# Optimization experiments

Hardware: AMD Instinct MI355X
Metric: run time of the kernel (lower is better)

Reference implementation:

```python
import jax, jax.numpy as jnp
import numpy as np

N = 768          # n_nuclei
EMB = 32         # embedding_dim
RBF = 32         # rbf_dim
CUTOFF = 10.0    # rbf_cutoff
MAXQ = 10        # max(charges)


def _edges(n):
    # fully-connected edge list exactly as in GNN.__call__
    senders = np.arange(n).repeat(n - 1)
    recv = np.arange(n)[None].repeat(n - 1, axis=0)
    recv = (recv + np.arange(n - 1)[:, None] + 1) % n
    return jnp.asarray(senders), jnp.asarray(recv.reshape(-1))


def _mlp2(x, w0, b0, w1, b1=None):
    # AutoMLP(out_dim, depth=2): Dense+silu, Dense (final_bias optional)
    h = jax.nn.silu(x @ w0 + b0)
    y = h @ w1
    return y if b1 is None else y + b1


def _seg_mean(vals, seg, n):
    s = jax.ops.segment_sum(vals, seg, num_segments=n, indices_are_sorted=True)
    c = jax.ops.segment_sum(jnp.ones((vals.shape[0], 1), vals.dtype), seg,
                            num_segments=n, indices_are_sorted=True)
    return s / jnp.maximum(c, 1.0)


def setup_inputs() -> dict:
    key = jax.random.key(0)
    ki = iter(jax.random.split(key, 48))

    def W(din, dout):
        return jax.random.normal(next(ki), (din, dout), jnp.float32) / np.sqrt(din).astype(np.float32)

    def b(d):
        return jax.random.normal(next(ki), (d,), jnp.float32) * 0.01

    return dict(
        nuclei=jax.random.normal(next(ki), (N, 3), jnp.float32) * 3.0,
        charges=jax.random.randint(next(ki), (N,), 0, MAXQ),
        f=(jnp.arange(RBF, dtype=jnp.float32) + 1.0) * jnp.pi,  # BesselRBF param init
        embed_table=jax.random.normal(next(ki), (MAXQ, EMB), jnp.float32),
        mp1_w0=W(96, 32), mp1_b0=b(32), mp1_w1=W(32, 32), mp1_b1=b(32),
        up1_w0=W(64, 64), up1_b0=b(64), up1_w1=W(64, 64), up1_b1=b(64),
        mp2_w0=W(160, 32), mp2_b0=b(32), mp2_w1=W(32, 32), mp2_b1=b(32),
        up2_w0=W(96, 64), up2_b0=b(64), up2_w1=W(64, 64), up2_b1=b(64),
        no_w0=W(160, 3), no_b0=b(3), no_w1=W(3, 3),
        no_embed=jax.random.normal(next(ki), (MAXQ, 3), jnp.float32) * 0.1,
        go_w0=W(160, 1), go_b0=b(1), go_w1=W(1, 1), go_b1=b(1),
    )


def reference(nuclei, charges, f, embed_table,
              mp1_w0, mp1_b0, mp1_w1, mp1_b1,
              up1_w0, up1_b0, up1_w1, up1_b1,
              mp2_w0, mp2_b0, mp2_w1, mp2_b1,
              up2_w0, up2_b0, up2_w1, up2_b1,
              no_w0, no_b0, no_w1, no_embed,
              go_w0, go_b0, go_w1, go_b1):
    nuclei = nuclei.reshape(-1, 3) @ jnp.eye(3, dtype=nuclei.dtype)  # constants 'axes'
    n = nuclei.shape[0]
    senders, receivers = _edges(n)

    # BesselRBF on pairwise distances
    d = jnp.linalg.norm(nuclei[senders] - nuclei[receivers], axis=-1)
    x_ext = d[:, None] + 1e-8
    e_embed = jnp.sqrt(2.0 / CUTOFF) * jnp.sin(f * x_ext / CUTOFF) / x_ext  # [E, RBF]

    n_embed = embed_table[charges]  # [N, EMB]
    embeddings = [n_embed]

    # layer 1: msg out 32, update out 64 (no residual: 32 != 64)
    edge_in = jnp.concatenate([n_embed[senders], n_embed[receivers], e_embed], axis=-1)
    msg = _seg_mean(_mlp2(edge_in, mp1_w0, mp1_b0, mp1_w1, mp1_b1), senders, n)
    upd = _mlp2(jnp.concatenate([n_embed, msg], axis=-1), up1_w0, up1_b0, up1_w1, up1_b1)
    n_embed = upd  # dims differ -> plain replacement
    embeddings.append(n_embed)

    # layer 2: msg out 32, update out 64 (residual: 64 == 64)
    edge_in = jnp.concatenate([n_embed[senders], n_embed[receivers], e_embed], axis=-1)
    msg = _seg_mean(_mlp2(edge_in, mp2_w0, mp2_b0, mp2_w1, mp2_b1), senders, n)
    upd = _mlp2(jnp.concatenate([n_embed, msg], axis=-1), up2_w0, up2_b0, up2_w1, up2_b1)
    n_embed = n_embed + upd
    embeddings.append(n_embed)

    agg = jnp.concatenate(embeddings, axis=-1)  # [N, 32+64+64=160]

    node_out = _mlp2(agg, no_w0, no_b0, no_w1) + no_embed[charges]  # [N, 3]
    global_out = _mlp2(jnp.mean(agg, axis=0), go_w0, go_b0, go_w1, go_b1)  # [1]
    return (node_out, global_out)
```

## Files before the change

kernel.cpp:

```cpp
#include <hip/hip_runtime.h>
#include <hip/hip_bf16.h>

typedef __hip_bfloat16 bf16;
typedef __attribute__((ext_vector_type(8))) short short8;
typedef __attribute__((ext_vector_type(4))) float float4v;

#define NN   768
#define NEPS 767

__device__ float g_emb1[NN*64];
__device__ float g_sa2[NN*32];
__device__ float g_sb2[NN*32];
__device__ float g_agg[640];
__device__ int   g_cnt;

struct Ptrs { const void* p[28]; };

__device__ __forceinline__ float b2f(bf16 v){ return __bfloat162float(v); }
__device__ __forceinline__ float LD(const void* p, int i, int f32){
  return f32 ? ((const float*)p)[i] : b2f(((const bf16*)p)[i]);
}
__device__ __forceinline__ int detect_f32(const void* f){
  float v = ((const float*)f)[0];
  return (fabsf(v - 3.14159265f) < 0.01f) ? 1 : 0;
}
__device__ __forceinline__ float fast_rcp(float x){ return __builtin_amdgcn_rcpf(x); }
__device__ __forceinline__ float silu_f(float p){ return p * fast_rcp(1.f + __expf(-p)); }
__device__ __forceinline__ unsigned short rne_bf16(float x){
  unsigned int b = __float_as_uint(x);
  return (unsigned short)((b + 0x7fffu + ((b >> 16) & 1u)) >> 16);
}

template<int NJ>
__device__ __forceinline__ float dotn(const void* wp, int base, int stride, int col,
                                      const float* x, int k0, int isf){
  float p = 0.f;
  if (isf){
    const float* f = (const float*)wp;
    #pragma unroll
    for (int j = 0; j < NJ; j++){ int k = k0 + j; p = fmaf(x[k], f[base + k*stride + col], p); }
  } else {
    const bf16* h = (const bf16*)wp;
    #pragma unroll
    for (int j = 0; j < NJ; j++){ int k = k0 + j; p = fmaf(x[k], b2f(h[base + k*stride + col]), p); }
  }
  return p;
}

__launch_bounds__(256)
__global__ void k_edge1(Ptrs P, const int* __restrict__ charges){
  __shared__ __align__(16) float pos[NN*3];
  __shared__ float etabL[320];
  __shared__ __align__(16) float w0F[2048];
  __shared__ float TBL[330];
  __shared__ int   chS[NN];
  __shared__ float w1L[1024];
  __shared__ float wsum[4][32], hsumL[32], msgL[32];
  __shared__ float catU[64], hU[64], e1U[64], part[256];

  int i = blockIdx.x, t = threadIdx.x;
  int w = t >> 6, lane = t & 63, q = lane >> 4, c = lane & 15;
  int isf = detect_f32(P.p[2]);

  if (i == 0){
    for (int idx = t; idx < 640; idx += 256) g_agg[idx] = 0.f;
    if (t == 0) g_cnt = 0;
  }
  for (int idx = t; idx < NN*3; idx += 256) pos[idx]   = LD(P.p[0], idx, isf);
  for (int idx = t; idx < 320;  idx += 256) etabL[idx] = LD(P.p[3], idx, isf);
  for (int idx = t; idx < 2048; idx += 256) w0F[idx]   = LD(P.p[4], idx, isf);
  for (int idx = t; idx < 1024; idx += 256) w1L[idx]   = LD(P.p[6], idx, isf);
  for (int idx = t; idx < NN;   idx += 256) chS[idx]   = charges[idx];

  short8 bfr0, bfr1;
  if (isf){
    const float* wp = (const float*)P.p[4];
    #pragma unroll
    for (int j = 0; j < 8; j++){
      int row = q*8 + j;
      bfr0[j] = (short)rne_bf16(wp[2048 + row*32 + c]);
      bfr1[j] = (short)rne_bf16(wp[2048 + row*32 + 16 + c]);
    }
  } else {
    const short* wp = (const short*)P.p[4];
    #pragma unroll
    for (int j = 0; j < 8; j++){
      int row = q*8 + j;
      bfr0[j] = wp[2048 + row*32 + c];
      bfr1[j] = wp[2048 + row*32 + 16 + c];
    }
  }
  float fj[8];
  #pragma unroll
  for (int j = 0; j < 8; j++) fj[j] = LD(P.p[2], q*8 + j, isf) * 0.1f;
  __syncthreads();

  for (int idx = t; idx < 320; idx += 256){
    int ch = idx >> 5, cc = idx & 31;
    float b = 0.f;
    #pragma unroll
    for (int k = 0; k < 32; k++) b = fmaf(etabL[ch*32 + k], w0F[1024 + k*32 + cc], b);
    TBL[ch*33 + cc] = b;
  }
  int chI = chS[i];
  float preB0 = LD(P.p[5], c, isf), preB1 = LD(P.p[5], 16 + c, isf);
  #pragma unroll
  for (int k = 0; k < 32; k++){
    float e = etabL[chI*32 + k];
    preB0 = fmaf(e, w0F[k*32 + c],      preB0);
    preB1 = fmaf(e, w0F[k*32 + 16 + c], preB1);
  }
  __syncthreads();

  float px = pos[i*3], py = pos[i*3+1], pz = pos[i*3+2];
  float xs[12], scv[12];
  #pragma unroll
  for (int s = 0; s < 12; s++){
    int el = (w + s*4)*16 + c;
    int ela = (el < NEPS) ? el : 0;
    int r = ela + (ela >= i);
    float dx = px - pos[r*3], dy = py - pos[r*3+1], dz = pz - pos[r*3+2];
    float d = sqrtf(fmaf(dx, dx, fmaf(dy, dy, dz*dz)));
    xs[s] = d + 1e-8f;
    scv[s] = 0.44721359549995793f * fast_rcp(xs[s]);
  }

  float sum0 = 0.f, sum1 = 0.f;
  #pragma unroll 4
  for (int s = 0; s < 12; s++){
    int tl = w + s*4;
    float sb0[4], sb1[4];
    #pragma unroll
    for (int p = 0; p < 4; p++){
      int el2 = tl*16 + q*4 + p;
      int e2a = (el2 < NEPS) ? el2 : 0;
      int r2 = e2a + (e2a >= i);
      int ch2 = chS[r2];
      sb0[p] = TBL[ch2*33 + c];
      sb1[p] = TBL[ch2*33 + 16 + c];
    }
    short8 af;
    #pragma unroll
    for (int j = 0; j < 8; j++) af[j] = (short)rne_bf16(scv[s] * __sinf(fj[j]*xs[s]));
    float4v z = {0.f, 0.f, 0.f, 0.f};
    float4v a0 = __builtin_amdgcn_mfma_f32_16x16x32_bf16(af, bfr0, z, 0, 0, 0);
    float4v a1 = __builtin_amdgcn_mfma_f32_16x16x32_bf16(af, bfr1, z, 0, 0, 0);
    #pragma unroll
    for (int p = 0; p < 4; p++){
      int el2 = tl*16 + q*4 + p;
      if (el2 < NEPS){
        sum0 += silu_f(a0[p] + preB0 + sb0[p]);
        sum1 += silu_f(a1[p] + preB1 + sb1[p]);
      }
    }
  }
  sum0 += __shfl_xor(sum0, 16); sum0 += __shfl_xor(sum0, 32);
  sum1 += __shfl_xor(sum1, 16); sum1 += __shfl_xor(sum1, 32);
  if (lane < 16){ wsum[w][lane] = sum0; wsum[w][16 + lane] = sum1; }
  __syncthreads();
  if (t < 32) hsumL[t] = wsum[0][t] + wsum[1][t] + wsum[2][t] + wsum[3][t];
  __syncthreads();
  if (t < 32){
    float y = 0.f;
    #pragma unroll
    for (int m = 0; m < 32; m++) y = fmaf(hsumL[m], w1L[m*32 + t], y);
    msgL[t] = y * (1.f/767.f) + LD(P.p[7], t, isf);
  }
  if (t < 32){ catU[t] = etabL[chI*32 + t]; catU[32 + t] = msgL[t]; }
  __syncthreads();

  int g = t >> 6, col = t & 63;
  part[t] = dotn<16>(P.p[8], 0, 64, col, catU, g*16, isf);
  __syncthreads();
  if (t < 64) hU[t] = silu_f(LD(P.p[9], t, isf) + part[t] + part[64+t] + part[128+t] + part[192+t]);
  __syncthreads();
  part[t] = dotn<16>(P.p[10], 0, 64, col, hU, g*16, isf);
  __syncthreads();
  if (t < 64){
    float y = LD(P.p[11], t, isf) + part[t] + part[64+t] + part[128+t] + part[192+t];
    e1U[t] = y;
    g_emb1[i*64 + t] = y;
  }
  __syncthreads();
  {
    int half = t >> 7, g2 = (t >> 5) & 3, c32 = t & 31;
    part[t] = dotn<16>(P.p[12], half*2048, 32, c32, e1U, g2*16, isf);
  }
  __syncthreads();
  if (t < 64){
    int half2 = t >> 5, cc = t & 31;
    float s = part[half2*128 + cc] + part[half2*128 + 32 + cc]
            + part[half2*128 + 64 + cc] + part[half2*128 + 96 + cc];
    if (half2 == 0) g_sa2[i*32 + cc] = s;
    else            g_sb2[i*32 + cc] = s;
  }
}

__launch_bounds__(256)
__global__ void k_edge2(Ptrs P, const int* __restrict__ charges, void* __restrict__ out){
  __shared__ __align__(16) float pos[NN*3];
  __shared__ float w1L[1024];
  __shared__ float noL[522];
  __shared__ float wsum[4][32], hsumL[32], msgL[32];
  __shared__ float catU[96], hU[64], aggL[160], h3L[3], part[256];
  __shared__ int lastL;

  int i = blockIdx.x, t = threadIdx.x;
  int w = t >> 6, lane = t & 63, q = lane >> 4, c = lane & 15;
  int isf = detect_f32(P.p[2]);

  for (int idx = t; idx < NN*3; idx += 256) pos[idx] = LD(P.p[0], idx, isf);
  for (int idx = t; idx < 1024; idx += 256) w1L[idx] = LD(P.p[14], idx, isf);
  for (int idx = t; idx < 522; idx += 256){
    float v;
    if      (idx < 480) v = LD(P.p[20], idx, isf);
    else if (idx < 483) v = LD(P.p[21], idx - 480, isf);
    else if (idx < 492) v = LD(P.p[22], idx - 483, isf);
    else                v = LD(P.p[23], idx - 492, isf);
    noL[idx] = v;
  }
  short8 cfr0, cfr1;
  if (isf){
    const float* wp = (const float*)P.p[12];
    #pragma unroll
    for (int j = 0; j < 8; j++){
      int row = q*8 + j;
      cfr0[j] = (short)rne_bf16(wp[4096 + row*32 + c]);
      cfr1[j] = (short)rne_bf16(wp[4096 + row*32 + 16 + c]);
    }
  } else {
    const short* wp = (const short*)P.p[12];
    #pragma unroll
    for (int j = 0; j < 8; j++){
      int row = q*8 + j;
      cfr0[j] = wp[4096 + row*32 + c];
      cfr1[j] = wp[4096 + row*32 + 16 + c];
    }
  }
  float fj[8];
  #pragma unroll
  for (int j = 0; j < 8; j++) fj[j] = LD(P.p[2], q*8 + j, isf) * 0.1f;
  float preC0 = g_sa2[i*32 + c]      + LD(P.p[13], c, isf);
  float preC1 = g_sa2[i*32 + 16 + c] + LD(P.p[13], 16 + c, isf);
  __syncthreads();

  float px = pos[i*3], py = pos[i*3+1], pz = pos[i*3+2];
  float xs[12], scv[12];
  #pragma unroll
  for (int s = 0; s < 12; s++){
    int el = (w + s*4)*16 + c;
    int ela = (el < NEPS) ? el : 0;
    int r = ela + (ela >= i);
    float dx = px - pos[r*3], dy = py - pos[r*3+1], dz = pz - pos[r*3+2];
    float d = sqrtf(fmaf(dx, dx, fmaf(dy, dy, dz*dz)));
    xs[s] = d + 1e-8f;
    scv[s] = 0.44721359549995793f * fast_rcp(xs[s]);
  }

  float sum0 = 0.f, sum1 = 0.f;
  #pragma unroll 4
  for (int s = 0; s < 12; s++){
    int tl = w + s*4;
    float sb0[4], sb1[4];
    #pragma unroll
    for (int p = 0; p < 4; p++){
      int el2 = tl*16 + q*4 + p;
      int e2a = (el2 < NEPS) ? el2 : 0;
      int r2 = e2a + (e2a >= i);
      sb0[p] = g_sb2[r2*32 + c];
      sb1[p] = g_sb2[r2*32 + 16 + c];
    }
    short8 af;
    #pragma unroll
    for (int j = 0; j < 8; j++) af[j] = (short)rne_bf16(scv[s] * __sinf(fj[j]*xs[s]));
    float4v z = {0.f, 0.f, 0.f, 0.f};
    float4v a0 = __builtin_amdgcn_mfma_f32_16x16x32_bf16(af, cfr0, z, 0, 0, 0);
    float4v a1 = __builtin_amdgcn_mfma_f32_16x16x32_bf16(af, cfr1, z, 0, 0, 0);
    #pragma unroll
    for (int p = 0; p < 4; p++){
      int el2 = tl*16 + q*4 + p;
      if (el2 < NEPS){
        sum0 += silu_f(a0[p] + preC0 + sb0[p]);
        sum1 += silu_f(a1[p] + preC1 + sb1[p]);
      }
    }
  }
  sum0 += __shfl_xor(sum0, 16); sum0 += __shfl_xor(sum0, 32);
  sum1 += __shfl_xor(sum1, 16); sum1 += __shfl_xor(sum1, 32);
  if (lane < 16){ wsum[w][lane] = sum0; wsum[w][16 + lane] = sum1; }
  __syncthreads();
  if (t < 32) hsumL[t] = wsum[0][t] + wsum[1][t] + wsum[2][t] + wsum[3][t];
  __syncthreads();
  if (t < 32){
    float y = 0.f;
    #pragma unroll
    for (int m = 0; m < 32; m++) y = fmaf(hsumL[m], w1L[m*32 + t], y);
    msgL[t] = y * (1.f/767.f) + LD(P.p[15], t, isf);
  }
  int chI = charges[i];
  if (t < 64) catU[t] = g_emb1[i*64 + t];
  if (t < 32){ catU[64 + t] = msgL[t]; aggL[t] = LD(P.p[3], chI*32 + t, isf); }
  __syncthreads();

  int g = t >> 6, col = t & 63;
  part[t] = dotn<24>(P.p[16], 0, 64, col, catU, g*24, isf);
  __syncthreads();
  if (t < 64) hU[t] = silu_f(LD(P.p[17], t, isf) + part[t] + part[64+t] + part[128+t] + part[192+t]);
  __syncthreads();
  part[t] = dotn<16>(P.p[18], 0, 64, col, hU, g*16, isf);
  __syncthreads();
  if (t < 64){
    float y = LD(P.p[19], t, isf) + part[t] + part[64+t] + part[128+t] + part[192+t];
    float e2 = catU[t] + y;
    aggL[32 + t] = catU[t];
    aggL[96 + t] = e2;
  }
  __syncthreads();
  if (t < 48){
    int chunk = t / 3, c3 = t - chunk*3;
    float p = 0.f;
    #pragma unroll
    for (int j = 0; j < 10; j++){ int k = chunk*10 + j; p = fmaf(aggL[k], noL[k*3 + c3], p); }
    part[t] = p;
  }
  __syncthreads();
  if (t < 3){
    float p = noL[480 + t];
    #pragma unroll
    for (int ch = 0; ch < 16; ch++) p += part[ch*3 + t];
    h3L[t] = silu_f(p);
  }
  __syncthreads();
  if (t < 3){
    float o = 0.f;
    #pragma unroll
    for (int m = 0; m < 3; m++) o = fmaf(h3L[m], noL[483 + m*3 + t], o);
    o += noL[492 + chI*3 + t];
    if (isf) ((float*)out)[i*3 + t] = o;
    else     ((bf16*)out)[i*3 + t] = __float2bfloat16(o);
  }
  if (t < 160) atomicAdd(&g_agg[(i & 3)*160 + t], aggL[t]);
  __syncthreads();
  if (t == 0) lastL = (atomicAdd(&g_cnt, 1) == NN - 1) ? 1 : 0;
  __syncthreads();
  if (lastL){
    float v = 0.f;
    if (t < 160){
      float s = atomicAdd(&g_agg[t], 0.f) + atomicAdd(&g_agg[160 + t], 0.f)
              + atomicAdd(&g_agg[320 + t], 0.f) + atomicAdd(&g_agg[480 + t], 0.f);
      v = s * (1.f/768.f) * LD(P.p[24], t, isf);
    }
    part[t] = v;
    __syncthreads();
    if (t == 0){
      float tot = 0.f;
      for (int k = 0; k < 160; k++) tot += part[k];
      float h = silu_f(tot + LD(P.p[25], 0, isf));
      float go = h * LD(P.p[26], 0, isf) + LD(P.p[27], 0, isf);
      if (isf) ((float*)out)[2304] = go;
      else     ((bf16*)out)[2304] = __float2bfloat16(go);
    }
  }
}

extern "C" void kernel_launch(void* const* d_in, const int* in_sizes, int n_in,
                              void* d_out, int out_size, void* d_ws, size_t ws_size,
                              hipStream_t stream) {
  Ptrs P;
  for (int k = 0; k < 28; k++) P.p[k] = d_in[k];
  const int* charges = (const int*)d_in[1];

  k_edge1<<<NN, 256, 0, stream>>>(P, charges);
  k_edge2<<<NN, 256, 0, stream>>>(P, charges, d_out);
}
```

Measured before the change: 173.8 us.

## Cache bf16 RBF fragments from edge1 in global memory and reuse in edge2

```diff
diff --git a/kernel.cpp b/kernel.cpp
--- a/kernel.cpp
+++ b/kernel.cpp
@@ -13,6 +13,7 @@
 __device__ float g_sb2[NN*32];
 __device__ float g_agg[640];
 __device__ int   g_cnt;
+__device__ short8 g_rbf[NN*48*64];
 
 struct Ptrs { const void* p[28]; };
 
@@ -142,6 +143,7 @@
     short8 af;
     #pragma unroll
     for (int j = 0; j < 8; j++) af[j] = (short)rne_bf16(scv[s] * __sinf(fj[j]*xs[s]));
+    g_rbf[(i*48 + tl)*64 + lane] = af;
     float4v z = {0.f, 0.f, 0.f, 0.f};
     float4v a0 = __builtin_amdgcn_mfma_f32_16x16x32_bf16(af, bfr0, z, 0, 0, 0);
     float4v a1 = __builtin_amdgcn_mfma_f32_16x16x32_bf16(af, bfr1, z, 0, 0, 0);
@@ -198,7 +200,6 @@
 
 __launch_bounds__(256)
 __global__ void k_edge2(Ptrs P, const int* __restrict__ charges, void* __restrict__ out){
-  __shared__ __align__(16) float pos[NN*3];
   __shared__ float w1L[1024];
   __shared__ float noL[522];
   __shared__ float wsum[4][32], hsumL[32], msgL[32];
@@ -209,7 +210,6 @@
   int w = t >> 6, lane = t & 63, q = lane >> 4, c = lane & 15;
   int isf = detect_f32(P.p[2]);
 
-  for (int idx = t; idx < NN*3; idx += 256) pos[idx] = LD(P.p[0], idx, isf);
   for (int idx = t; idx < 1024; idx += 256) w1L[idx] = LD(P.p[14], idx, isf);
   for (int idx = t; idx < 522; idx += 256){
     float v;
@@ -237,52 +237,52 @@
       cfr1[j] = wp[4096 + row*32 + 16 + c];
     }
   }
-  float fj[8];
-  #pragma unroll
-  for (int j = 0; j < 8; j++) fj[j] = LD(P.p[2], q*8 + j, isf) * 0.1f;
   float preC0 = g_sa2[i*32 + c]      + LD(P.p[13], c, isf);
   float preC1 = g_sa2[i*32 + 16 + c] + LD(P.p[13], 16 + c, isf);
-  __syncthreads();
-
-  float px = pos[i*3], py = pos[i*3+1], pz = pos[i*3+2];
-  float xs[12], scv[12];
-  #pragma unroll
-  for (int s = 0; s < 12; s++){
-    int el = (w + s*4)*16 + c;
-    int ela = (el < NEPS) ? el : 0;
-    int r = ela + (ela >= i);
-    float dx = px - pos[r*3], dy = py - pos[r*3+1], dz = pz - pos[r*3+2];
-    float d = sqrtf(fmaf(dx, dx, fmaf(dy, dy, dz*dz)));
-    xs[s] = d + 1e-8f;
-    scv[s] = 0.44721359549995793f * fast_rcp(xs[s]);
-  }
 
   float sum0 = 0.f, sum1 = 0.f;
-  #pragma unroll 4
+  short8 afA = g_rbf[(i*48 + w)*64 + lane];
+  float sbA0[4], sbA1[4];
+  #pragma unroll
+  for (int p = 0; p < 4; p++){
+    int el2 = w*16 + q*4 + p;
+    int e2a = (el2 < NEPS) ? el2 : 0;
+    int r2 = e2a + (e2a >= i);
+    sbA0[p] = g_sb2[r2*32 + c];
+    sbA1[p] = g_sb2[r2*32 + 16 + c];
+  }
+  #pragma unroll
   for (int s = 0; s < 12; s++){
     int tl = w + s*4;
-    float sb0[4], sb1[4];
-    #pragma unroll
-    for (int p = 0; p < 4; p++){
-      int el2 = tl*16 + q*4 + p;
-      int e2a = (el2 < NEPS) ? el2 : 0;
-      int r2 = e2a + (e2a >= i);
-      sb0[p] = g_sb2[r2*32 + c];
-      sb1[p] = g_sb2[r2*32 + 16 + c];
-    }
-    short8 af;
-    #pragma unroll
-    for (int j = 0; j < 8; j++) af[j] = (short)rne_bf16(scv[s] * __sinf(fj[j]*xs[s]));
+    short8 afB;
+    float sbB0[4], sbB1[4];
+    if (s < 11){
+      int tn = tl + 4;
+      afB = g_rbf[(i*48 + tn)*64 + lane];
+      #pragma unroll
+      for (int p = 0; p < 4; p++){
+        int el2 = tn*16 + q*4 + p;
+        int e2a = (el2 < NEPS) ? el2 : 0;
+        int r2 = e2a + (e2a >= i);
+        sbB0[p] = g_sb2[r2*32 + c];
+        sbB1[p] = g_sb2[r2*32 + 16 + c];
+      }
+    }
     float4v z = {0.f, 0.f, 0.f, 0.f};
-    float4v a0 = __builtin_amdgcn_mfma_f32_16x16x32_bf16(af, cfr0, z, 0, 0, 0);
-    float4v a1 = __builtin_amdgcn_mfma_f32_16x16x32_bf16(af, cfr1, z, 0, 0, 0);
+    float4v a0 = __builtin_amdgcn_mfma_f32_16x16x32_bf16(afA, cfr0, z, 0, 0, 0);
+    float4v a1 = __builtin_amdgcn_mfma_f32_16x16x32_bf16(afA, cfr1, z, 0, 0, 0);
     #pragma unroll
     for (int p = 0; p < 4; p++){
       int el2 = tl*16 + q*4 + p;
       if (el2 < NEPS){
-        sum0 += silu_f(a0[p] + preC0 + sb0[p]);
-        sum1 += silu_f(a1[p] + preC1 + sb1[p]);
+        sum0 += silu_f(a0[p] + preC0 + sbA0[p]);
+        sum1 += silu_f(a1[p] + preC1 + sbA1[p]);
       }
+    }
+    if (s < 11){
+      afA = afB;
+      #pragma unroll
+      for (int p = 0; p < 4; p++){ sbA0[p] = sbB0[p]; sbA1[p] = sbB1[p]; }
     }
   }
   sum0 += __shfl_xor(sum0, 16); sum0 += __shfl_xor(sum0, 32);
```

Measured after the change: 165.5 us. 1.05x faster.
